# Optimization experiments

Measured on AMD Instinct MI355X. Metric: run time of the kernel, lower is better.

## Reference

```python
import jax, jax.numpy as jnp
import numpy as np

PERIOD = 24
NUM_ITERATIONS = 2


def _window_size():
    w = max(3, PERIOD // 2)  # 12
    if w % 2 == 0:
        w += 1  # 13
    return w


def moving_average(s, w):
    # s: [N, L]; replicate-pad by w//2 on each side, then width-w mean conv ('VALID')
    pad = w // 2
    sp = jnp.pad(s, ((0, 0), (pad, pad)), mode='edge')[:, None, :]  # [N,1,L+2*pad]
    k = jnp.ones((1, 1, w), s.dtype) / w
    y = jax.lax.conv_general_dilated(sp, k, window_strides=(1,), padding='VALID',
                                     dimension_numbers=('NCH', 'OIH', 'NCH'))
    return y[:, 0, :]  # [N, L]


def extract_seasonal(d):
    # d: [N, L] with L a multiple of PERIOD. Strided indices i, i+P, ... correspond
    # to reshape [N, C, P] with fixed last axis; median over cycles, broadcast back.
    N, L = d.shape
    C = L // PERIOD
    sub = d.reshape(N, C, PERIOD)
    med = jnp.median(sub, axis=1)  # [N, P] (C=121 is odd -> matches torch.median)
    return jnp.broadcast_to(med[:, None, :], (N, C, PERIOD)).reshape(N, L)


def setup_inputs() -> dict:
    key = jax.random.key(0)
    x = jax.random.normal(key, (64, 2904, 207), dtype=jnp.float32)
    return {"x": x}


def reference(x):
    # x: [B, L, F] -> process all features at once as [B*F, L]
    B, L, F = x.shape
    s = jnp.transpose(x, (0, 2, 1)).reshape(B * F, L)
    w = _window_size()
    trend = moving_average(s, w)
    for _ in range(NUM_ITERATIONS):
        seasonal = extract_seasonal(s - trend)
        trend = moving_average(s - seasonal, w)
    residual = s - trend - seasonal

    def unflatten(a):
        return jnp.transpose(a.reshape(B, F, L), (0, 2, 1))  # [B, L, F]

    return unflatten(trend), unflatten(seasonal), unflatten(residual)
```

## Files before the change

kernel.cpp:

```cpp
#include <hip/hip_runtime.h>

#define LROW    2904
#define PERIOD  24
#define CYC     121
#define NF      207
#define NB      64
#define NROWS   13248
#define NSLOT   61
#define KPAD    256
#define KSTRIDE (NSLOT * KPAD)
#define NT      256
#define LTILE   24
#define NLT     121
#define K2GRID  (NB * NLT)
#define K2CHUNK (K2GRID / 8)
#define R13     (1.f / 13.f)

typedef unsigned short us2 __attribute__((ext_vector_type(2)));

__device__ __forceinline__ int clampi(int i) {
    return i < 0 ? 0 : (i >= LROW ? LROW - 1 : i);
}
__device__ __forceinline__ unsigned quantk(float d) {
    int ki = (int)fmaf(d, 4096.f, 32768.f);
    ki = ki < 0 ? 0 : (ki > 65535 ? 65535 : ki);
    return (unsigned)ki;
}
__device__ __forceinline__ float dqmid(unsigned k) {
    return ((float)(int)k - 32767.5f) * (1.f / 4096.f);
}

__device__ __forceinline__ unsigned sel60(const unsigned (&K)[NSLOT]) {
    unsigned T = 0;
    const us2 one2 = __builtin_bit_cast(us2, 0x00010001u);
    for (int bit = 15; bit >= 0; --bit) {
        unsigned Tp = T | (1u << bit);
        unsigned tm32 = (Tp - 1u) | ((Tp - 1u) << 16);
        us2 tm2 = __builtin_bit_cast(us2, tm32);
        us2 acc = __builtin_bit_cast(us2, 0u);
        #pragma unroll
        for (int s = 0; s < NSLOT; ++s) {
            us2 kv = __builtin_bit_cast(us2, K[s]);
            us2 dd = __builtin_elementwise_sub_sat(kv, tm2);
            us2 mm = __builtin_elementwise_min(dd, one2);
            acc = acc + mm;
        }
        unsigned a = __builtin_bit_cast(unsigned, acc);
        int cnt = (int)(a & 0xFFFFu) + (int)(a >> 16);
        if (cnt >= 62) T = Tp;
    }
    return T;
}

__global__ __launch_bounds__(256) void k_keys(const float* __restrict__ x,
                                              unsigned* __restrict__ keys) {
    __shared__ float T[62 * NF];
    const int b  = blockIdx.x;
    const int cp = blockIdx.y;
    const int fl = threadIdx.x;
    const int fe = fl < NF ? fl : NF - 1;
    const int l0 = cp * 48;
    const float* xb = x + (size_t)b * (LROW * NF);
    unsigned* kb = keys + ((size_t)b * PERIOD * NSLOT + cp) * KPAD + fl;

    if (cp != 0 && cp != 60) {
        const float2* s2 = (const float2*)(xb + (size_t)(l0 - 8) * NF);
        float2* t2 = (float2*)T;
        for (int i = fl; i < 62 * NF / 2; i += NT) t2[i] = s2[i];
    } else {
        for (int i = fl; i < 62 * NF; i += NT) {
            int lr = i / NF, ff = i - lr * NF;
            T[i] = xb[(size_t)clampi(l0 - 8 + lr) * NF + ff];
        }
    }
    __syncthreads();

    float r[13];
    #pragma unroll
    for (int i = 0; i < 13; ++i) r[i] = T[(i + 1) * NF + fe];
    float sum = ((r[0] + r[1]) + (r[2] + r[3])) + ((r[4] + r[5]) + (r[6] + r[7]))
              + ((r[8] + r[9]) + (r[10] + r[11])) + r[12];

    if (cp < 60) {
        unsigned pend[PERIOD];
        #pragma unroll
        for (int j = 0; j < 48; ++j) {
            float xn = T[(j + 14) * NF + fe];
            sum += xn - r[0];
            unsigned k = quantk(r[7] - sum * R13);
            if (j < 24) pend[j] = k;
            else kb[(size_t)(j - 24) * KSTRIDE] = pend[j - 24] | (k << 16);
            #pragma unroll
            for (int i = 0; i < 12; ++i) r[i] = r[i + 1];
            r[12] = xn;
        }
    } else {
        #pragma unroll
        for (int j = 0; j < 24; ++j) {
            float xn = T[(j + 14) * NF + fe];
            sum += xn - r[0];
            unsigned k = quantk(r[7] - sum * R13);
            kb[(size_t)j * KSTRIDE] = k | 0xFFFF0000u;
            #pragma unroll
            for (int i = 0; i < 12; ++i) r[i] = r[i + 1];
            r[12] = xn;
        }
    }
}

__global__ __launch_bounds__(256) void k_med0(const unsigned* __restrict__ keys,
                                              unsigned short* __restrict__ med0key) {
    const int d  = blockIdx.x;
    const int bp = (d & 7) * 192 + (d >> 3);
    const int fl = threadIdx.x;
    unsigned K[NSLOT];
    const unsigned* kp = keys + (size_t)bp * KSTRIDE + fl;
    #pragma unroll
    for (int s = 0; s < NSLOT; ++s) K[s] = kp[(size_t)s * KPAD];
    unsigned T = sel60(K);
    if (fl < NF) med0key[(size_t)bp * NF + fl] = (unsigned short)T;
}

__global__ __launch_bounds__(256) void k_edge(const unsigned* __restrict__ keys,
                                              const unsigned short* __restrict__ med0key,
                                              float* __restrict__ medBedge) {
    const int d  = blockIdx.x;
    const int bj = (d & 7) * 48 + (d >> 3);
    const int b = bj / 6, j = bj - 6 * b;
    const int fl = threadIdx.x;
    const int fe = fl < NF ? fl : NF - 1;

    float m0[PERIOD];
    #pragma unroll
    for (int p = 0; p < PERIOD; ++p)
        m0[p] = dqmid(med0key[(size_t)(b * PERIOD + p) * NF + fe]);

    float wA = 0.f, wB = 0.f, weA = 0.f, weB = 0.f;
    #pragma unroll
    for (int jj = 0; jj < 6; ++jj) if (jj == j) {
        #pragma unroll
        for (int t = 0; t < 13; ++t) {
            wA += m0[(jj + 18 + t) % 24];
            wB += m0[(jj + 12 + t) % 24];
        }
        #pragma unroll
        for (int t = -6; t <= 6; ++t) {
            int aa = jj + t;       if (aa < 0)  aa = 0;
            int bb = 18 + jj + t;  if (bb > 23) bb = 23;
            weA += m0[aa];
            weB += m0[bb];
        }
    }

    unsigned K[NSLOT];
    {
        const unsigned* kp = keys + (size_t)(b * PERIOD + j) * KSTRIDE + fl;
        #pragma unroll
        for (int s = 0; s < NSLOT; ++s) K[s] = kp[(size_t)s * KPAD];
        unsigned kn = quantk(dqmid(K[0] & 0xFFFFu) + (weA - wA) * R13);
        K[0] = (K[0] & 0xFFFF0000u) | kn;
        unsigned T = sel60(K);
        if (fl < NF) medBedge[(size_t)(b * 12 + j) * NF + fl] = dqmid(T) + wA * R13;
    }
    {
        const unsigned* kp = keys + (size_t)(b * PERIOD + 18 + j) * KSTRIDE + fl;
        #pragma unroll
        for (int s = 0; s < NSLOT; ++s) K[s] = kp[(size_t)s * KPAD];
        unsigned kn = quantk(dqmid(K[60] & 0xFFFFu) + (weB - wB) * R13);
        K[60] = (K[60] & 0xFFFF0000u) | kn;
        unsigned T = sel60(K);
        if (fl < NF) medBedge[(size_t)(b * 12 + 6 + j) * NF + fl] = dqmid(T) + wB * R13;
    }
}

__global__ __launch_bounds__(64) void k_final(const unsigned short* __restrict__ med0key,
                                              const float* __restrict__ medBedge,
                                              float* __restrict__ wsTab) {
    const int blk = blockIdx.x;
    const int b = blk >> 2, ft = blk & 3;
    const int lane = threadIdx.x;
    const int f = ft * 64 + lane;
    const int fe = f < NF ? f : NF - 1;

    float m0[PERIOD], mB[PERIOD];
    #pragma unroll
    for (int p = 0; p < PERIOD; ++p)
        m0[p] = dqmid(med0key[(size_t)(b * PERIOD + p) * NF + fe]);
    float W0[PERIOD];
    {
        float s = 0.f;
        #pragma unroll
        for (int t = 0; t < 13; ++t) s += m0[t];
        W0[0] = s;
        #pragma unroll
        for (int q = 1; q < PERIOD; ++q)
            W0[q] = W0[q - 1] + m0[(q + 12) % 24] - m0[q - 1];
    }
    #pragma unroll
    for (int e = 0; e < 12; ++e) {
        int p = (e < 6) ? e : e + 12;
        mB[p] = medBedge[(size_t)(b * 12 + e) * NF + fe];
    }
    #pragma unroll
    for (int p = 6; p < 18; ++p) mB[p] = m0[p] + W0[p - 6] * R13;
    float W1[PERIOD];
    {
        float s = 0.f;
        #pragma unroll
        for (int t = 0; t < 13; ++t) s += mB[t];
        W1[0] = s;
        #pragma unroll
        for (int q = 1; q < PERIOD; ++q)
            W1[q] = W1[q - 1] + mB[(q + 12) % 24] - mB[q - 1];
    }
    if (f < NF) {
        #pragma unroll
        for (int p = 0; p < PERIOD; ++p) {
            wsTab[((size_t)b * 48 + p) * NF + f]      = mB[p];
            wsTab[((size_t)b * 48 + 24 + p) * NF + f] = W1[p];
        }
    }
}

__global__ __launch_bounds__(NT, 5) void stl_outputs(const float* __restrict__ x,
                                                     const float* __restrict__ ws,
                                                     float* __restrict__ out) {
    __shared__ float T[(LTILE + 12) * NF];

    const int d   = blockIdx.x;
    const int blk = (d & 7) * K2CHUNK + (d >> 3);
    const int b  = blk / NLT;
    const int kk = blk - b * NLT;
    const int l0 = kk * LTILE;
    const int t  = threadIdx.x;
    const float* xb = x + (size_t)b * (LROW * NF);

    if (kk != 0 && kk != NLT - 1) {
        const float2* s2 = (const float2*)(xb + (size_t)(l0 - 6) * NF);
        float2* t2 = (float2*)T;
        for (int i = t; i < (LTILE + 12) * NF / 2; i += NT) t2[i] = s2[i];
    } else {
        for (int i = t; i < (LTILE + 12) * NF; i += NT) {
            int lr = i / NF;
            int ff = i - lr * NF;
            T[i] = xb[(size_t)clampi(l0 - 6 + lr) * NF + ff];
        }
    }
    __syncthreads();

    if (t < NF) {
        float lm[PERIOD], wt[PERIOD];
        const float* wrow = ws + (size_t)b * 48 * NF + t;
        #pragma unroll
        for (int i = 0; i < PERIOD; ++i) lm[i] = wrow[i * NF];
        #pragma unroll
        for (int i = 0; i < PERIOD; ++i) wt[i] = wrow[(PERIOD + i) * NF];

        float s13 = 0.f;
        #pragma unroll
        for (int r = 0; r < 13; ++r) s13 += T[r * NF + t];

        const bool edgeLo = (kk == 0), edgeHi = (kk == NLT - 1);
        const size_t S = (size_t)NROWS * LROW;
        const size_t obase = (size_t)b * (LROW * NF) + (size_t)l0 * NF + (size_t)t;

        #pragma unroll
        for (int j = 0; j < LTILE; ++j) {
            float W = wt[(j + 18) % 24];
            if (edgeLo && j < 6) {
                float w = 0.f;
                #pragma unroll
                for (int jj = -6; jj <= 6; ++jj) { int m = j + jj; if (m < 0) m = 0; w += lm[m]; }
                W = w;
            }
            if (edgeHi && j >= 18) {
                float w = 0.f;
                #pragma unroll
                for (int jj = -6; jj <= 6; ++jj) { int m = j + jj; if (m > 23) m = 23; w += lm[m]; }
                W = w;
            }
            float tr = (s13 - W) * R13;
            float se = lm[j];
            float re = T[(j + 6) * NF + t] - tr - se;
            size_t o = obase + (size_t)(j * NF);
            __builtin_nontemporal_store(tr, &out[o]);
            __builtin_nontemporal_store(se, &out[S + o]);
            __builtin_nontemporal_store(re, &out[2 * S + o]);
            if (j < LTILE - 1)
                s13 += T[(j + 13) * NF + t] - T[j * NF + t];
        }
    }
}

extern "C" void kernel_launch(void* const* d_in, const int* in_sizes, int n_in,
                              void* d_out, int out_size, void* d_ws, size_t ws_size,
                              hipStream_t stream) {
    const float* x = (const float*)d_in[0];
    float* out = (float*)d_out;
    float* wsf = (float*)d_ws;
    (void)in_sizes; (void)n_in; (void)out_size; (void)ws_size;

    float*    wsTab    = wsf;
    unsigned* keys     = (unsigned*)(wsf + 635904);
    float*    medBedge = wsf + 635904 + 23986176;
    unsigned short* med0key = (unsigned short*)(wsf + 635904 + 23986176 + 158976);

    hipLaunchKernelGGL(k_keys,   dim3(NB, NSLOT), dim3(NT), 0, stream, x, keys);
    hipLaunchKernelGGL(k_med0,   dim3(NB * PERIOD), dim3(NT), 0, stream, keys, med0key);
    hipLaunchKernelGGL(k_edge,   dim3(NB * 6), dim3(NT), 0, stream, keys, med0key, medBedge);
    hipLaunchKernelGGL(k_final,  dim3(NB * 4), dim3(64), 0, stream, med0key, medBedge, wsTab);
    hipLaunchKernelGGL(stl_outputs, dim3(K2GRID), dim3(NT), 0, stream, x, wsTab, out);
}
```

Measured before the change: 357.1 us.

## Shrink key padding, split edge medians per phase, fold final table into outputs

Cuts the key-array row padding from 256 to 208 floats so less workspace is written and read. The edge-median kernel now handles one phase per block, twelve per batch. It uses a single selection pass at an adjusted rank threshold and fixes up the result relative to the known first-pass median, instead of running a full median select per edge. The separate k_final table kernel is removed and its window sums are recomputed per thread inside stl_outputs, saving a launch and a round-trip through global memory at the cost of extra per-thread arithmetic.

```diff
diff --git a/kernel.cpp b/kernel.cpp
--- a/kernel.cpp
+++ b/kernel.cpp
@@ -4,11 +4,10 @@
 #define PERIOD  24
 #define CYC     121
 #define NF      207
+#define KF      208
 #define NB      64
 #define NROWS   13248
 #define NSLOT   61
-#define KPAD    256
-#define KSTRIDE (NSLOT * KPAD)
 #define NT      256
 #define LTILE   24
 #define NLT     121
@@ -30,7 +29,7 @@
     return ((float)(int)k - 32767.5f) * (1.f / 4096.f);
 }
 
-__device__ __forceinline__ unsigned sel60(const unsigned (&K)[NSLOT]) {
+__device__ __forceinline__ unsigned selN(const unsigned (&K)[NSLOT], int thr) {
     unsigned T = 0;
     const us2 one2 = __builtin_bit_cast(us2, 0x00010001u);
     for (int bit = 15; bit >= 0; --bit) {
@@ -47,7 +46,7 @@
         }
         unsigned a = __builtin_bit_cast(unsigned, acc);
         int cnt = (int)(a & 0xFFFFu) + (int)(a >> 16);
-        if (cnt >= 62) T = Tp;
+        if (cnt >= thr) T = Tp;
     }
     return T;
 }
@@ -61,7 +60,7 @@
     const int fe = fl < NF ? fl : NF - 1;
     const int l0 = cp * 48;
     const float* xb = x + (size_t)b * (LROW * NF);
-    unsigned* kb = keys + ((size_t)b * PERIOD * NSLOT + cp) * KPAD + fl;
+    unsigned* kb = keys + ((size_t)b * PERIOD * NSLOT + cp) * KF + fl;
 
     if (cp != 0 && cp != 60) {
         const float2* s2 = (const float2*)(xb + (size_t)(l0 - 8) * NF);
@@ -78,8 +77,8 @@
     float r[13];
     #pragma unroll
     for (int i = 0; i < 13; ++i) r[i] = T[(i + 1) * NF + fe];
-    float sum = ((r[0] + r[1]) + (r[2] + r[3])) + ((r[4] + r[5]) + (r[6] + r[7]))
-              + ((r[8] + r[9]) + (r[10] + r[11])) + r[12];
+    float sum = ((r[0]+r[1])+(r[2]+r[3]))+((r[4]+r[5])+(r[6]+r[7]))
+              + ((r[8]+r[9])+(r[10]+r[11])) + r[12];
 
     if (cp < 60) {
         unsigned pend[PERIOD];
@@ -89,7 +88,8 @@
             sum += xn - r[0];
             unsigned k = quantk(r[7] - sum * R13);
             if (j < 24) pend[j] = k;
-            else kb[(size_t)(j - 24) * KSTRIDE] = pend[j - 24] | (k << 16);
+            else if (fl < KF)
+                kb[(size_t)(j - 24) * (NSLOT * KF)] = pend[j - 24] | (k << 16);
             #pragma unroll
             for (int i = 0; i < 12; ++i) r[i] = r[i + 1];
             r[12] = xn;
@@ -100,7 +100,8 @@
             float xn = T[(j + 14) * NF + fe];
             sum += xn - r[0];
             unsigned k = quantk(r[7] - sum * R13);
-            kb[(size_t)j * KSTRIDE] = k | 0xFFFF0000u;
+            if (fl < KF)
+                kb[(size_t)j * (NSLOT * KF)] = k | 0xFFFF0000u;
             #pragma unroll
             for (int i = 0; i < 12; ++i) r[i] = r[i + 1];
             r[12] = xn;
@@ -109,121 +110,68 @@
 }
 
 __global__ __launch_bounds__(256) void k_med0(const unsigned* __restrict__ keys,
-                                              unsigned short* __restrict__ med0key) {
+                                              unsigned short* __restrict__ m0key) {
     const int d  = blockIdx.x;
     const int bp = (d & 7) * 192 + (d >> 3);
     const int fl = threadIdx.x;
+    const int fx = fl < KF ? fl : KF - 1;
     unsigned K[NSLOT];
-    const unsigned* kp = keys + (size_t)bp * KSTRIDE + fl;
-    #pragma unroll
-    for (int s = 0; s < NSLOT; ++s) K[s] = kp[(size_t)s * KPAD];
-    unsigned T = sel60(K);
-    if (fl < NF) med0key[(size_t)bp * NF + fl] = (unsigned short)T;
-}
-
-__global__ __launch_bounds__(256) void k_edge(const unsigned* __restrict__ keys,
-                                              const unsigned short* __restrict__ med0key,
-                                              float* __restrict__ medBedge) {
+    const unsigned* kp = keys + (size_t)bp * NSLOT * KF + fx;
+    #pragma unroll
+    for (int s = 0; s < NSLOT; ++s) K[s] = kp[(size_t)s * KF];
+    unsigned T = selN(K, 62);
+    if (fl < KF) m0key[(size_t)bp * KF + fl] = (unsigned short)T;
+}
+
+__global__ __launch_bounds__(256) void k_edge2(const unsigned* __restrict__ keys,
+                                               const unsigned short* __restrict__ m0key,
+                                               float* __restrict__ medBedge) {
     const int d  = blockIdx.x;
-    const int bj = (d & 7) * 48 + (d >> 3);
-    const int b = bj / 6, j = bj - 6 * b;
+    const int be = (d & 7) * 96 + (d >> 3);
+    const int b = be / 12, e = be - 12 * b;
+    const int p = (e < 6) ? e : e + 12;
     const int fl = threadIdx.x;
-    const int fe = fl < NF ? fl : NF - 1;
+    const int fx = fl < KF ? fl : KF - 1;
 
     float m0[PERIOD];
     #pragma unroll
-    for (int p = 0; p < PERIOD; ++p)
-        m0[p] = dqmid(med0key[(size_t)(b * PERIOD + p) * NF + fe]);
-
-    float wA = 0.f, wB = 0.f, weA = 0.f, weB = 0.f;
-    #pragma unroll
-    for (int jj = 0; jj < 6; ++jj) if (jj == j) {
-        #pragma unroll
-        for (int t = 0; t < 13; ++t) {
-            wA += m0[(jj + 18 + t) % 24];
-            wB += m0[(jj + 12 + t) % 24];
-        }
+    for (int q = 0; q < PERIOD; ++q)
+        m0[q] = dqmid(m0key[(size_t)(b * PERIOD + q) * KF + fx]);
+
+    float wph = 0.f, we = 0.f;
+    #pragma unroll
+    for (int ee = 0; ee < 12; ++ee) if (ee == e) {
+        const int pp = (ee < 6) ? ee : ee + 12;
+        #pragma unroll
+        for (int t = 0; t < 13; ++t) wph += m0[(pp + 18 + t) % 24];
         #pragma unroll
         for (int t = -6; t <= 6; ++t) {
-            int aa = jj + t;       if (aa < 0)  aa = 0;
-            int bb = 18 + jj + t;  if (bb > 23) bb = 23;
-            weA += m0[aa];
-            weB += m0[bb];
+            int aa = pp + t; if (aa < 0) aa = 0; if (aa > 23) aa = 23;
+            we += m0[aa];
         }
     }
 
     unsigned K[NSLOT];
-    {
-        const unsigned* kp = keys + (size_t)(b * PERIOD + j) * KSTRIDE + fl;
-        #pragma unroll
-        for (int s = 0; s < NSLOT; ++s) K[s] = kp[(size_t)s * KPAD];
-        unsigned kn = quantk(dqmid(K[0] & 0xFFFFu) + (weA - wA) * R13);
-        K[0] = (K[0] & 0xFFFF0000u) | kn;
-        unsigned T = sel60(K);
-        if (fl < NF) medBedge[(size_t)(b * 12 + j) * NF + fl] = dqmid(T) + wA * R13;
-    }
-    {
-        const unsigned* kp = keys + (size_t)(b * PERIOD + 18 + j) * KSTRIDE + fl;
-        #pragma unroll
-        for (int s = 0; s < NSLOT; ++s) K[s] = kp[(size_t)s * KPAD];
-        unsigned kn = quantk(dqmid(K[60] & 0xFFFFu) + (weB - wB) * R13);
-        K[60] = (K[60] & 0xFFFF0000u) | kn;
-        unsigned T = sel60(K);
-        if (fl < NF) medBedge[(size_t)(b * 12 + 6 + j) * NF + fl] = dqmid(T) + wB * R13;
-    }
-}
-
-__global__ __launch_bounds__(64) void k_final(const unsigned short* __restrict__ med0key,
-                                              const float* __restrict__ medBedge,
-                                              float* __restrict__ wsTab) {
-    const int blk = blockIdx.x;
-    const int b = blk >> 2, ft = blk & 3;
-    const int lane = threadIdx.x;
-    const int f = ft * 64 + lane;
-    const int fe = f < NF ? f : NF - 1;
-
-    float m0[PERIOD], mB[PERIOD];
-    #pragma unroll
-    for (int p = 0; p < PERIOD; ++p)
-        m0[p] = dqmid(med0key[(size_t)(b * PERIOD + p) * NF + fe]);
-    float W0[PERIOD];
-    {
-        float s = 0.f;
-        #pragma unroll
-        for (int t = 0; t < 13; ++t) s += m0[t];
-        W0[0] = s;
-        #pragma unroll
-        for (int q = 1; q < PERIOD; ++q)
-            W0[q] = W0[q - 1] + m0[(q + 12) % 24] - m0[q - 1];
-    }
-    #pragma unroll
-    for (int e = 0; e < 12; ++e) {
-        int p = (e < 6) ? e : e + 12;
-        mB[p] = medBedge[(size_t)(b * 12 + e) * NF + fe];
-    }
-    #pragma unroll
-    for (int p = 6; p < 18; ++p) mB[p] = m0[p] + W0[p - 6] * R13;
-    float W1[PERIOD];
-    {
-        float s = 0.f;
-        #pragma unroll
-        for (int t = 0; t < 13; ++t) s += mB[t];
-        W1[0] = s;
-        #pragma unroll
-        for (int q = 1; q < PERIOD; ++q)
-            W1[q] = W1[q - 1] + mB[(q + 12) % 24] - mB[q - 1];
-    }
-    if (f < NF) {
-        #pragma unroll
-        for (int p = 0; p < PERIOD; ++p) {
-            wsTab[((size_t)b * 48 + p) * NF + f]      = mB[p];
-            wsTab[((size_t)b * 48 + 24 + p) * NF + f] = W1[p];
-        }
-    }
+    const unsigned* kp = keys + (size_t)(b * PERIOD + p) * NSLOT * KF + fx;
+    #pragma unroll
+    for (int s = 0; s < NSLOT; ++s) K[s] = kp[(size_t)s * KF];
+
+    unsigned m = (unsigned)m0key[(size_t)(b * PERIOD + p) * KF + fx];
+    unsigned xk = ((p < 6) ? K[0] : K[60]) & 0xFFFFu;
+    unsigned y = quantk(dqmid(xk) + (we - wph) * R13);
+
+    int thr = (y > m) ? 61 : 63;
+    unsigned v = selN(K, thr);
+    bool up = (y > m) && (xk <= m);
+    bool dn = (y < m) && (xk >= m);
+    unsigned nm = up ? (y < v ? y : v) : (dn ? (y > v ? y : v) : m);
+    if (fl < KF)
+        medBedge[(size_t)(b * 12 + e) * KF + fl] = dqmid(nm) + wph * R13;
 }
 
 __global__ __launch_bounds__(NT, 5) void stl_outputs(const float* __restrict__ x,
-                                                     const float* __restrict__ ws,
+                                                     const unsigned short* __restrict__ m0key,
+                                                     const float* __restrict__ medBedge,
                                                      float* __restrict__ out) {
     __shared__ float T[(LTILE + 12) * NF];
 
@@ -249,12 +197,38 @@
     __syncthreads();
 
     if (t < NF) {
-        float lm[PERIOD], wt[PERIOD];
-        const float* wrow = ws + (size_t)b * 48 * NF + t;
-        #pragma unroll
-        for (int i = 0; i < PERIOD; ++i) lm[i] = wrow[i * NF];
-        #pragma unroll
-        for (int i = 0; i < PERIOD; ++i) wt[i] = wrow[(PERIOD + i) * NF];
+        float m0[PERIOD];
+        #pragma unroll
+        for (int q = 0; q < PERIOD; ++q)
+            m0[q] = dqmid(m0key[(size_t)(b * PERIOD + q) * KF + t]);
+        float W0[PERIOD];
+        {
+            float s = 0.f;
+            #pragma unroll
+            for (int q = 0; q < 13; ++q) s += m0[q];
+            W0[0] = s;
+            #pragma unroll
+            for (int q = 1; q < PERIOD; ++q)
+                W0[q] = W0[q - 1] + m0[(q + 12) % 24] - m0[q - 1];
+        }
+        float lm[PERIOD];
+        #pragma unroll
+        for (int e = 0; e < 12; ++e) {
+            int p = (e < 6) ? e : e + 12;
+            lm[p] = medBedge[(size_t)(b * 12 + e) * KF + t];
+        }
+        #pragma unroll
+        for (int p = 6; p < 18; ++p) lm[p] = m0[p] + W0[p - 6] * R13;
+        float wt[PERIOD];
+        {
+            float s = 0.f;
+            #pragma unroll
+            for (int q = 0; q < 13; ++q) s += lm[q];
+            wt[0] = s;
+            #pragma unroll
+            for (int q = 1; q < PERIOD; ++q)
+                wt[q] = wt[q - 1] + lm[(q + 12) % 24] - lm[q - 1];
+        }
 
         float s13 = 0.f;
         #pragma unroll
@@ -300,14 +274,13 @@
     float* wsf = (float*)d_ws;
     (void)in_sizes; (void)n_in; (void)out_size; (void)ws_size;
 
-    float*    wsTab    = wsf;
-    unsigned* keys     = (unsigned*)(wsf + 635904);
-    float*    medBedge = wsf + 635904 + 23986176;
-    unsigned short* med0key = (unsigned short*)(wsf + 635904 + 23986176 + 158976);
+    unsigned*       keys     = (unsigned*)wsf;
+    unsigned short* m0key    = (unsigned short*)(wsf + 19489792);
+    float*          medBedge = wsf + 19489792 + 159744;
 
     hipLaunchKernelGGL(k_keys,   dim3(NB, NSLOT), dim3(NT), 0, stream, x, keys);
-    hipLaunchKernelGGL(k_med0,   dim3(NB * PERIOD), dim3(NT), 0, stream, keys, med0key);
-    hipLaunchKernelGGL(k_edge,   dim3(NB * 6), dim3(NT), 0, stream, keys, med0key, medBedge);
-    hipLaunchKernelGGL(k_final,  dim3(NB * 4), dim3(64), 0, stream, med0key, medBedge, wsTab);
-    hipLaunchKernelGGL(stl_outputs, dim3(K2GRID), dim3(NT), 0, stream, x, wsTab, out);
-}
+    hipLaunchKernelGGL(k_med0,   dim3(NB * PERIOD), dim3(NT), 0, stream, keys, m0key);
+    hipLaunchKernelGGL(k_edge2,  dim3(NB * 12), dim3(NT), 0, stream, keys, m0key, medBedge);
+    hipLaunchKernelGGL(stl_outputs, dim3(K2GRID), dim3(NT), 0, stream,
+                       x, m0key, medBedge, out);
+}
```

Result: faster. 336.9 us (-5.7%).
